# Performance work log

Measured on AMD Instinct MI355X. Metric: run time of the kernel, lower is better.

## Reference

```python
import jax, jax.numpy as jnp
import numpy as np
from jax import lax

STRIDE = 16
SCALES = (8.0, 16.0, 32.0)
RATIOS = (0.5, 1.0, 2.0)
PRE_NMS = 6000
POST_NMS = 300
NMS_THRESH = 0.7
MIN_SIZE = 16.0
DN = ('NCHW', 'OIHW', 'NCHW')


def _base_anchors():
    # 9 base anchors centered at (STRIDE/2, STRIDE/2), (ymin,xmin,ymax,xmax)
    c = STRIDE / 2.0
    rows = []
    for r in RATIOS:
        for s in SCALES:
            h = STRIDE * s * np.sqrt(r)
            w = STRIDE * s * np.sqrt(1.0 / r)
            rows.append([c - h / 2, c - w / 2, c + h / 2, c + w / 2])
    return jnp.asarray(np.array(rows, np.float32))


def _all_anchors(wdim, hdim):
    # shift base anchors over the (w, h) feature grid, matching permute(0,2,3,1) flatten order
    sy = jnp.arange(wdim, dtype=jnp.float32) * STRIDE
    sx = jnp.arange(hdim, dtype=jnp.float32) * STRIDE
    yy, xx = jnp.meshgrid(sy, sx, indexing='ij')
    shifts = jnp.stack([yy, xx, yy, xx], axis=-1).reshape(-1, 4)  # [w*h, 4]
    return (shifts[:, None, :] + _base_anchors()[None, :, :]).reshape(-1, 4)  # [w*h*9, 4]


def _conv(x, W, b, pad):
    y = lax.conv_general_dilated(x, W, (1, 1), pad, dimension_numbers=DN)
    return y + b[None, :, None, None]


def _nms_fixed(boxes, keep):
    # sequential greedy NMS over score-sorted boxes; returns POST_NMS boxes (zero padded)
    y1, x1, y2, x2 = boxes[:, 0], boxes[:, 1], boxes[:, 2], boxes[:, 3]
    areas = (y2 - y1) * (x2 - x1)
    N = boxes.shape[0]
    idxs = jnp.arange(N)

    def body(i, keep):
        yy1 = jnp.maximum(y1[i], y1)
        xx1 = jnp.maximum(x1[i], x1)
        yy2 = jnp.minimum(y2[i], y2)
        xx2 = jnp.minimum(x2[i], x2)
        inter = jnp.maximum(yy2 - yy1, 0.0) * jnp.maximum(xx2 - xx1, 0.0)
        iou = inter / (areas[i] + areas - inter + 1e-12)
        suppress = (iou > NMS_THRESH) & (idxs > i) & keep[i]
        return keep & ~suppress

    keep = lax.fori_loop(0, N, body, keep)
    rank = jnp.cumsum(keep) - 1
    slot = jnp.where(keep & (rank < POST_NMS), rank, POST_NMS)  # overflow slot
    out = jnp.zeros((POST_NMS + 1, 4), boxes.dtype).at[slot].set(boxes)
    return out[:POST_NMS]


def _proposals(loc, score_fg, anchors, img_h, img_w):
    ah = anchors[:, 2] - anchors[:, 0]
    aw = anchors[:, 3] - anchors[:, 1]
    acy = anchors[:, 0] + 0.5 * ah
    acx = anchors[:, 1] + 0.5 * aw
    cy = loc[:, 0] * ah + acy
    cx = loc[:, 1] * aw + acx
    h = jnp.exp(loc[:, 2]) * ah
    w = jnp.exp(loc[:, 3]) * aw
    boxes = jnp.stack([cy - 0.5 * h, cx - 0.5 * w, cy + 0.5 * h, cx + 0.5 * w], axis=-1)
    hi = jnp.array([img_h, img_w, img_h, img_w], dtype=boxes.dtype)
    boxes = jnp.clip(boxes, 0.0, hi)
    hs = boxes[:, 2] - boxes[:, 0]
    ws = boxes[:, 3] - boxes[:, 1]
    valid = (hs >= MIN_SIZE) & (ws >= MIN_SIZE)
    sc = jnp.where(valid, score_fg, -jnp.inf)
    top_sc, top_idx = lax.top_k(sc, PRE_NMS)
    cand = boxes[top_idx]
    return _nms_fixed(cand, jnp.isfinite(top_sc))


def setup_inputs() -> dict:
    key = jax.random.key(0)
    k = jax.random.split(key, 4)
    return {
        'base_feature_map': jax.random.normal(k[0], (8, 512, 50, 50), jnp.float32),
        'W_conv': jax.random.normal(k[1], (512, 512, 3, 3), jnp.float32) * 0.01,
        'b_conv': jnp.zeros((512,), jnp.float32),
        'W_cls': jax.random.normal(k[2], (18, 512, 1, 1), jnp.float32) * 0.01,
        'b_cls': jnp.zeros((18,), jnp.float32),
        'W_reg': jax.random.normal(k[3], (36, 512, 1, 1), jnp.float32) * 0.01,
        'b_reg': jnp.zeros((36,), jnp.float32),
        'img_h': 800,
        'img_w': 800,
    }


def reference(base_feature_map, W_conv, b_conv, W_cls, b_cls, W_reg, b_reg, img_h, img_w):
    n, _, w, h = base_feature_map.shape
    anchors = _all_anchors(w, h)  # [w*h*9, 4]
    x = jax.nn.relu(_conv(base_feature_map, W_conv, b_conv, 'SAME'))
    rpn_locs = _conv(x, W_reg, b_reg, 'VALID').transpose(0, 2, 3, 1).reshape(n, -1, 4)
    rpn_scores = _conv(x, W_cls, b_cls, 'VALID').transpose(0, 2, 3, 1).reshape(n, -1, 2)
    fg = jax.nn.softmax(rpn_scores[0], axis=-1)[:, 1]
    rois = _proposals(rpn_locs[0], fg, anchors, float(img_h), float(img_w))
    return rpn_locs, rpn_scores, anchors, rois
```

## Files before the change

### kernel.cpp

```cpp
#include <hip/hip_runtime.h>
#include <cstdint>
#include <math.h>

typedef unsigned int u32;
typedef unsigned long long u64;
typedef __attribute__((ext_vector_type(8))) short short8v;
typedef __attribute__((ext_vector_type(4))) float f32x4;

#define N_BATCH 8
#define C_IN    512
#define PX      2500
#define KDIM    4608
#define NA      22500
#define PRE_NMS 6000
#define POST_NMS 300

#define OUT_SCORES 720000
#define OUT_ANCH   1080000
#define OUT_ROIS   1170000

#define WS_X     0
#define WS_SCORE 10240000
#define WS_BOX   10262500
#define WS_LIST  10352500
#define WS_CAND  10364500
#define WS_META  10388500
#define WS_WP    10388608
#define WS_XP    12747904
#define WS_END   22987904

__device__ inline u32 rne_hi16(float f) {
    u32 u = __float_as_uint(f);
    return (u + 0x7FFFu + ((u >> 16) & 1u)) >> 16;
}

__global__ __launch_bounds__(256) void k_splitW(const float* __restrict__ Wc,
                                                u32* __restrict__ WP) {
    int o = blockIdx.x * 256 + threadIdx.x;
    if (o >= 512 * KDIM) return;
    int ci_in = o & 31;
    int tmp   = o >> 5;
    int r     = tmp % 9;
    int cc    = tmp / 9;
    int co    = cc >> 4;
    int cig   = cc & 15;
    int ci    = cig * 32 + ci_in;
    float f = Wc[(size_t)co * KDIM + ci * 9 + r];
    u32 rh  = rne_hi16(f);
    float d = f - __uint_as_float(rh << 16);
    u32 rl  = rne_hi16(d);
    WP[o] = (rh << 16) | rl;
}

__global__ __launch_bounds__(256) void k_splitX(const float* __restrict__ in,
                                                u32* __restrict__ XP) {
    int o = blockIdx.x * 256 + threadIdx.x;
    if (o >= N_BATCH * C_IN * PX) return;
    float f = in[o];
    u32 rh  = rne_hi16(f);
    float d = f - __uint_as_float(rh << 16);
    u32 rl  = rne_hi16(d);
    XP[o] = (rh << 16) | rl;
}

__global__ __launch_bounds__(256) void k_conv3(const float* __restrict__ in,
                                               const u32* __restrict__ XP,
                                               const u32* __restrict__ WP,
                                               const float* __restrict__ bc,
                                               float* __restrict__ xout) {
    __shared__ unsigned short AsH[128][40];
    __shared__ unsigned short AsL[128][40];
    __shared__ unsigned short BsH[128][40];
    __shared__ unsigned short BsL[128][40];

    int b  = blockIdx.x;
    int n  = b & 7;
    int q  = b >> 3;
    int cb = q & 3;
    int pt = q >> 2;
    int t  = threadIdx.x;
    int lane = t & 63;
    int w  = t >> 6;
    int wr = w >> 1, wc = w & 1;
    int px0 = pt * 128, co0 = cb * 128;
    const float* inN = in + (size_t)n * C_IN * PX;
    const u32*   XPn = XP ? (XP + (size_t)n * C_IN * PX) : nullptr;

    int sco = t >> 1;
    int skb = (t & 1) << 4;
    int spx = t & 127;
    int skk = (t >> 7) << 4;
    int gpx = px0 + spx;
    int sy  = gpx / 50;
    int sx  = gpx - sy * 50;
    bool pxok = (gpx < PX);
    const u32* wpA = WP + (size_t)(co0 + sco) * KDIM + skb;

    f32x4 acc[4][4];
#pragma unroll
    for (int i = 0; i < 4; ++i)
#pragma unroll
        for (int j = 0; j < 4; ++j) acc[i][j] = (f32x4)0.f;

    const int ro = lane & 15;
    const int g8 = (lane >> 4) << 3;

    for (int cig = 0; cig < 16; ++cig) {
        int ci0 = cig << 5;
        for (int r = 0; r < 9; ++r) {
            int kstep = cig * 9 + r;
            {
                const u32* wp = wpA + kstep * 32;
                u32 uu[16];
                *(uint4*)&uu[0]  = *(const uint4*)(wp);
                *(uint4*)&uu[4]  = *(const uint4*)(wp + 4);
                *(uint4*)&uu[8]  = *(const uint4*)(wp + 8);
                *(uint4*)&uu[12] = *(const uint4*)(wp + 12);
                short8v v0, v1, u0, u1;
#pragma unroll
                for (int e = 0; e < 8; ++e) {
                    v0[e] = (short)(uu[e] >> 16);
                    v1[e] = (short)(uu[8 + e] >> 16);
                    u0[e] = (short)(uu[e] & 0xFFFFu);
                    u1[e] = (short)(uu[8 + e] & 0xFFFFu);
                }
                *(short8v*)&AsH[sco][skb]     = v0;
                *(short8v*)&AsH[sco][skb + 8] = v1;
                *(short8v*)&AsL[sco][skb]     = u0;
                *(short8v*)&AsL[sco][skb + 8] = u1;
            }
            {
                int ry = (r * 11) >> 5;
                int dy = ry - 1;
                int dx = r - ry * 3 - 1;
                int iy = sy + dy, ix = sx + dx;
                bool valid = pxok && ((unsigned)iy < 50u) && ((unsigned)ix < 50u);
                int off = iy * 50 + ix;
                short8v v0, v1, u0, u1;
                if (XPn) {
                    const u32* bp = XPn + (size_t)(ci0 + skk) * PX + off;
                    u32 uu[16];
#pragma unroll
                    for (int it = 0; it < 16; ++it)
                        uu[it] = valid ? bp[it * PX] : 0u;
#pragma unroll
                    for (int e = 0; e < 8; ++e) {
                        v0[e] = (short)(uu[e] >> 16);
                        v1[e] = (short)(uu[8 + e] >> 16);
                        u0[e] = (short)(uu[e] & 0xFFFFu);
                        u1[e] = (short)(uu[8 + e] & 0xFFFFu);
                    }
                } else {
                    const float* bp = inN + (size_t)(ci0 + skk) * PX + off;
                    float bv[16];
#pragma unroll
                    for (int it = 0; it < 16; ++it)
                        bv[it] = valid ? bp[it * PX] : 0.f;
#pragma unroll
                    for (int e = 0; e < 8; ++e) {
                        u32 ha = rne_hi16(bv[e]);
                        u32 hb = rne_hi16(bv[8 + e]);
                        float da = bv[e]     - __uint_as_float(ha << 16);
                        float db = bv[8 + e] - __uint_as_float(hb << 16);
                        v0[e] = (short)ha;
                        v1[e] = (short)hb;
                        u0[e] = (short)rne_hi16(da);
                        u1[e] = (short)rne_hi16(db);
                    }
                }
                *(short8v*)&BsH[spx][skk]     = v0;
                *(short8v*)&BsH[spx][skk + 8] = v1;
                *(short8v*)&BsL[spx][skk]     = u0;
                *(short8v*)&BsL[spx][skk + 8] = u1;
            }
            __syncthreads();

            short8v aH[4], aL[4], bH[4], bL[4];
#pragma unroll
            for (int s = 0; s < 4; ++s) {
                aH[s] = *(const short8v*)&AsH[wr * 64 + s * 16 + ro][g8];
                aL[s] = *(const short8v*)&AsL[wr * 64 + s * 16 + ro][g8];
                bH[s] = *(const short8v*)&BsH[wc * 64 + s * 16 + ro][g8];
                bL[s] = *(const short8v*)&BsL[wc * 64 + s * 16 + ro][g8];
            }
#pragma unroll
            for (int i = 0; i < 4; ++i)
#pragma unroll
                for (int j = 0; j < 4; ++j) {
                    acc[i][j] = __builtin_amdgcn_mfma_f32_16x16x32_bf16(aH[i], bH[j], acc[i][j], 0, 0, 0);
                    acc[i][j] = __builtin_amdgcn_mfma_f32_16x16x32_bf16(aH[i], bL[j], acc[i][j], 0, 0, 0);
                    acc[i][j] = __builtin_amdgcn_mfma_f32_16x16x32_bf16(aL[i], bH[j], acc[i][j], 0, 0, 0);
                }
            __syncthreads();
        }
    }

    int coB  = co0 + wr * 64;
    int pxB  = px0 + wc * 64 + ro;
    int rowg = (lane >> 4) << 2;
#pragma unroll
    for (int i = 0; i < 4; ++i) {
#pragma unroll
        for (int rg = 0; rg < 4; ++rg) {
            int co = coB + i * 16 + rowg + rg;
            float bias = bc[co];
            float* dst = xout + ((size_t)n * C_IN + co) * PX;
#pragma unroll
            for (int j = 0; j < 4; ++j) {
                int px = pxB + j * 16;
                if (px < PX) dst[px] = fmaxf(acc[i][j][rg] + bias, 0.f);
            }
        }
    }
}

__global__ __launch_bounds__(256) void k_heads(const float* __restrict__ x,
                                               const float* __restrict__ Wreg,
                                               const float* __restrict__ breg,
                                               const float* __restrict__ Wcls,
                                               const float* __restrict__ bcls,
                                               float* __restrict__ out) {
    __shared__ float As[32][68];
    __shared__ float Bs[32][132];
    int b  = blockIdx.x;
    int pt = b % 20, n = b / 20;
    int t  = threadIdx.x;
    int tx = t & 15, ty = t >> 4;
    int px0 = pt * 128;
    float acc[4][8];
#pragma unroll
    for (int i = 0; i < 4; ++i)
#pragma unroll
        for (int j = 0; j < 8; ++j) acc[i][j] = 0.f;

    for (int k0 = 0; k0 < 512; k0 += 32) {
        {
            int c   = t >> 2;
            int kkb = (t & 3) << 3;
            const float* src = nullptr;
            if (c < 36)      src = Wreg + (size_t)c * 512 + k0 + kkb;
            else if (c < 54) src = Wcls + (size_t)(c - 36) * 512 + k0 + kkb;
#pragma unroll
            for (int q = 0; q < 2; ++q) {
                float4 w = src ? *(const float4*)(src + q * 4) : make_float4(0, 0, 0, 0);
                As[kkb + q * 4 + 0][c] = w.x;
                As[kkb + q * 4 + 1][c] = w.y;
                As[kkb + q * 4 + 2][c] = w.z;
                As[kkb + q * 4 + 3][c] = w.w;
            }
        }
        {
            int pxl = t & 127;
            int kk0 = (t >> 7) << 4;
            int px  = px0 + pxl;
#pragma unroll
            for (int it = 0; it < 16; ++it) {
                int kk = kk0 + it;
                float v = 0.f;
                if (px < PX) v = x[((size_t)n * 512 + k0 + kk) * PX + px];
                Bs[kk][pxl] = v;
            }
        }
        __syncthreads();
#pragma unroll 8
        for (int kk = 0; kk < 32; ++kk) {
            float a[4], bb[8];
            *(float4*)&a[0]  = *(const float4*)&As[kk][ty * 4];
            *(float4*)&bb[0] = *(const float4*)&Bs[kk][tx * 8];
            *(float4*)&bb[4] = *(const float4*)&Bs[kk][tx * 8 + 4];
#pragma unroll
            for (int i = 0; i < 4; ++i)
#pragma unroll
                for (int j = 0; j < 8; ++j)
                    acc[i][j] = fmaf(a[i], bb[j], acc[i][j]);
        }
        __syncthreads();
    }
    int pxb = px0 + tx * 8;
#pragma unroll
    for (int i = 0; i < 4; ++i) {
        int c = ty * 4 + i;
        if (c >= 54) continue;
        float bias = (c < 36) ? breg[c] : bcls[c - 36];
        for (int j = 0; j < 8; ++j) {
            int px = pxb + j;
            if (px >= PX) break;
            float v = acc[i][j] + bias;
            if (c < 36)
                out[(size_t)n * 90000 + (size_t)px * 36 + c] = v;
            else
                out[OUT_SCORES + (size_t)n * 45000 + (size_t)px * 18 + (c - 36)] = v;
        }
    }
}

__device__ inline float readDim(const void* p) {
    int v = *(const int*)p;
    if (v > 0 && v <= 100000) return (float)v;
    return *(const float*)p;
}

__global__ __launch_bounds__(256) void k_decode(float* __restrict__ dout,
                                                float* __restrict__ ws,
                                                const void* pih, const void* piw) {
    int idx = blockIdx.x * 256 + threadIdx.x;
    if (idx >= NA) return;
    float imgH = readDim(pih), imgW = readDim(piw);
    int a  = idx % 9;
    int px = idx / 9;
    int y = px / 50, x = px - y * 50;
    const float ratios[3] = {0.5f, 1.f, 2.f};
    const float scales[3] = {8.f, 16.f, 32.f};
    float r = ratios[a / 3], s = scales[a % 3];
    float hh = 16.f * s * sqrtf(r);
    float wv = 16.f * s * sqrtf(1.f / r);
    float ay1 = y * 16.f + 8.f - 0.5f * hh;
    float ax1 = x * 16.f + 8.f - 0.5f * wv;
    float ay2 = y * 16.f + 8.f + 0.5f * hh;
    float ax2 = x * 16.f + 8.f + 0.5f * wv;
    *(float4*)(dout + OUT_ANCH + (size_t)idx * 4) = make_float4(ay1, ax1, ay2, ax2);

    float4 loc = *(const float4*)(dout + (size_t)idx * 4);
    float s0 = dout[OUT_SCORES + (size_t)idx * 2];
    float s1 = dout[OUT_SCORES + (size_t)idx * 2 + 1];
    float fg = 1.f / (1.f + expf(s0 - s1));
    float ah = ay2 - ay1, aw = ax2 - ax1;
    float acy = ay1 + 0.5f * ah, acx = ax1 + 0.5f * aw;
    float cy = loc.x * ah + acy;
    float cx = loc.y * aw + acx;
    float bh = expf(loc.z) * ah;
    float bw = expf(loc.w) * aw;
    float b0 = cy - 0.5f * bh, b1 = cx - 0.5f * bw;
    float b2 = cy + 0.5f * bh, b3 = cx + 0.5f * bw;
    b0 = fminf(fmaxf(b0, 0.f), imgH);
    b1 = fminf(fmaxf(b1, 0.f), imgW);
    b2 = fminf(fmaxf(b2, 0.f), imgH);
    b3 = fminf(fmaxf(b3, 0.f), imgW);
    bool valid = ((b2 - b0) >= 16.f) && ((b3 - b1) >= 16.f);
    ws[WS_SCORE + idx] = valid ? fg : -INFINITY;
    *(float4*)(ws + WS_BOX + (size_t)idx * 4) = make_float4(b0, b1, b2, b3);
}

__device__ inline u32 fkey(float s) {
    u32 u = __float_as_uint(s);
    return (u & 0x80000000u) ? ~u : (u | 0x80000000u);
}

__global__ __launch_bounds__(1024) void k_select(const float* __restrict__ score,
                                                 u64* __restrict__ list,
                                                 int* __restrict__ meta) {
    __shared__ u32 hist[4096];
    __shared__ int sB1, sB2, sB3, sM3, sNeed, sV;
    __shared__ u32 sT32;
    __shared__ int cHi, cTie;
    int t = threadIdx.x;
    const int NT = 1024;

    for (int i = t; i < 4096; i += NT) hist[i] = 0;
    __syncthreads();
    for (int i = t; i < NA; i += NT) atomicAdd(&hist[fkey(score[i]) >> 20], 1u);
    __syncthreads();
    for (int off = 1; off < 4096; off <<= 1) {
        u32 v[4]; int c = 0;
        for (int bb = t; bb < 4096; bb += NT) { v[c++] = hist[bb] + ((bb + off < 4096) ? hist[bb + off] : 0u); }
        __syncthreads();
        c = 0;
        for (int bb = t; bb < 4096; bb += NT) hist[bb] = v[c++];
        __syncthreads();
    }
    for (int bb = t; bb < 4096; bb += NT) {
        u32 Sb  = hist[bb];
        u32 Sb1 = (bb < 4095) ? hist[bb + 1] : 0u;
        if (Sb >= PRE_NMS && Sb1 < PRE_NMS) sB1 = bb;
    }
    if (t == 0) sV = (int)hist[2048];
    __syncthreads();
    int B1 = sB1;
    int m1 = (B1 < 4095) ? (int)hist[B1 + 1] : 0;
    int V  = sV;
    __syncthreads();

    for (int i = t; i < 4096; i += NT) hist[i] = 0;
    __syncthreads();
    for (int i = t; i < NA; i += NT) {
        u32 key = fkey(score[i]);
        if ((int)(key >> 20) == B1) atomicAdd(&hist[(key >> 8) & 0xFFFu], 1u);
    }
    __syncthreads();
    for (int off = 1; off < 4096; off <<= 1) {
        u32 v[4]; int c = 0;
        for (int bb = t; bb < 4096; bb += NT) { v[c++] = hist[bb] + ((bb + off < 4096) ? hist[bb + off] : 0u); }
        __syncthreads();
        c = 0;
        for (int bb = t; bb < 4096; bb += NT) hist[bb] = v[c++];
        __syncthreads();
    }
    for (int bb = t; bb < 4096; bb += NT) {
        int Sb  = m1 + (int)hist[bb];
        int Sb1 = m1 + (int)((bb < 4095) ? hist[bb + 1] : 0u);
        if (Sb >= PRE_NMS && Sb1 < PRE_NMS) sB2 = bb;
    }
    __syncthreads();
    int B2 = sB2;
    int m2 = m1 + (int)((B2 < 4095) ? hist[B2 + 1] : 0u);
    u32 P24 = ((u32)B1 << 12) | (u32)B2;
    __syncthreads();

    for (int i = t; i < 256; i += NT) hist[i] = 0;
    __syncthreads();
    for (int i = t; i < NA; i += NT) {
        u32 key = fkey(score[i]);
        if ((key >> 8) == P24) atomicAdd(&hist[key & 0xFFu], 1u);
    }
    __syncthreads();
    for (int off = 1; off < 256; off <<= 1) {
        u32 v[1]; int c = 0;
        for (int bb = t; bb < 256; bb += NT) { v[c++] = hist[bb] + ((bb + off < 256) ? hist[bb + off] : 0u); }
        __syncthreads();
        c = 0;
        for (int bb = t; bb < 256; bb += NT) hist[bb] = v[c++];
        __syncthreads();
    }
    for (int bb = t; bb < 256; bb += NT) {
        int Sb  = m2 + (int)hist[bb];
        int Sb1 = m2 + (int)((bb < 255) ? hist[bb + 1] : 0u);
        if (Sb >= PRE_NMS && Sb1 < PRE_NMS) {
            sB3   = bb;
            sM3   = m2 + (int)((bb < 255) ? hist[bb + 1] : 0u);
            sNeed = PRE_NMS - sM3;
            sT32  = (P24 << 8) | (u32)bb;
        }
    }
    if (t == 0) { cHi = 0; cTie = 0; meta[0] = (V < PRE_NMS) ? V : PRE_NMS; }
    __syncthreads();
    int m3 = sM3, need = sNeed;
    u32 T32 = sT32;

    for (int i = t; i < NA; i += NT) {
        u32 key = fkey(score[i]);
        u64 comp = ((u64)key << 32) | (u64)(0xFFFFFFFFu - (u32)i);
        if (key > T32) {
            int p = atomicAdd(&cHi, 1);
            list[p] = comp;
        } else if (key == T32) {
            int p = atomicAdd(&cTie, 1);
            if (p < need) list[m3 + p] = comp;
        }
    }
}

__global__ __launch_bounds__(1024) void k_sort(u64* __restrict__ list,
                                               const float* __restrict__ boxes,
                                               float* __restrict__ cand) {
    __shared__ u64 sb[8192];
    int t = threadIdx.x;
    for (int i = t; i < 8192; i += 1024) sb[i] = (i < PRE_NMS) ? list[i] : 0ull;
    __syncthreads();
    for (int k = 2; k <= 8192; k <<= 1) {
        for (int j = k >> 1; j > 0; j >>= 1) {
            for (int i = t; i < 8192; i += 1024) {
                int ixj = i ^ j;
                if (ixj > i) {
                    u64 a = sb[i], b = sb[ixj];
                    bool desc = ((i & k) == 0);
                    if (desc ? (a < b) : (a > b)) { sb[i] = b; sb[ixj] = a; }
                }
            }
            __syncthreads();
        }
    }
    for (int e = t; e < PRE_NMS; e += 1024) {
        u32 idx = 0xFFFFFFFFu - (u32)sb[e];
        float4 bx = *(const float4*)(boxes + (size_t)idx * 4);
        *(float4*)(cand + (size_t)e * 4) = bx;
    }
}

__global__ __launch_bounds__(256) void k_nms(const float* __restrict__ cand,
                                             const int* __restrict__ meta,
                                             float* __restrict__ rois) {
    __shared__ float kb[POST_NMS][4];
    __shared__ u64 supArr[4];
    int t = threadIdx.x;
    int lane = t & 63, wid = t >> 6;
    int keepN = meta[0];
    int kept = 0;

    for (int c0 = 0; c0 < PRE_NMS && kept < POST_NMS; c0 += 64) {
        int i = c0 + lane;
        float y1 = 0, x1 = 0, y2 = 0, x2 = 0;
        bool elig = (i < keepN);
        if (i < PRE_NMS) {
            float4 bx = *(const float4*)(cand + (size_t)i * 4);
            y1 = bx.x; x1 = bx.y; y2 = bx.z; x2 = bx.w;
        } else {
            elig = false;
        }
        float area = (y2 - y1) * (x2 - x1);

        bool supA = false;
        for (int jj = wid; jj < kept; jj += 4) {
            float ky1 = kb[jj][0], kx1 = kb[jj][1], ky2 = kb[jj][2], kx2 = kb[jj][3];
            float yy1 = fmaxf(ky1, y1), xx1 = fmaxf(kx1, x1);
            float yy2 = fminf(ky2, y2), xx2 = fminf(kx2, x2);
            float inter = fmaxf(yy2 - yy1, 0.f) * fmaxf(xx2 - xx1, 0.f);
            float karea = (ky2 - ky1) * (kx2 - kx1);
            float iou = inter / (karea + area - inter + 1e-12f);
            if (iou > 0.7f) { supA = true; break; }
        }
        supArr[wid] = __ballot(supA);
        __syncthreads();
        u64 sup = supArr[0] | supArr[1] | supArr[2] | supArr[3];
        u64 eligMask = __ballot(elig);

        for (int s = 0; s < 64; ++s) {
            if (kept >= POST_NMS) break;
            if (!((eligMask >> s) & 1ull)) continue;
            if ((sup >> s) & 1ull) continue;
            float sy1 = __shfl(y1, s), sx1 = __shfl(x1, s);
            float sy2 = __shfl(y2, s), sx2 = __shfl(x2, s);
            float sar = __shfl(area, s);
            if (wid == 0 && lane == s) {
                kb[kept][0] = y1; kb[kept][1] = x1; kb[kept][2] = y2; kb[kept][3] = x2;
                *(float4*)(rois + (size_t)kept * 4) = make_float4(y1, x1, y2, x2);
            }
            float yy1 = fmaxf(sy1, y1), xx1 = fmaxf(sx1, x1);
            float yy2 = fminf(sy2, y2), xx2 = fminf(sx2, x2);
            float inter = fmaxf(yy2 - yy1, 0.f) * fmaxf(xx2 - xx1, 0.f);
            float iou = inter / (sar + area - inter + 1e-12f);
            bool kill = (lane > s) && (iou > 0.7f);
            sup |= __ballot(kill);
            kept++;
        }
        __syncthreads();
    }
    for (int r = kept * 4 + t; r < POST_NMS * 4; r += 256) rois[r] = 0.f;
}

extern "C" void kernel_launch(void* const* d_in, const int* in_sizes, int n_in,
                              void* d_out, int out_size, void* d_ws, size_t ws_size,
                              hipStream_t stream) {
    const float* feat = (const float*)d_in[0];
    const float* Wc   = (const float*)d_in[1];
    const float* bc   = (const float*)d_in[2];
    const float* Wcls = (const float*)d_in[3];
    const float* bcls = (const float*)d_in[4];
    const float* Wreg = (const float*)d_in[5];
    const float* breg = (const float*)d_in[6];
    const void* pih   = d_in[7];
    const void* piw   = d_in[8];
    float* out = (float*)d_out;
    float* ws  = (float*)d_ws;

    u32* WP   = (u32*)(ws + WS_WP);
    u64* list = (u64*)(ws + WS_LIST);
    int* meta = (int*)(ws + WS_META);

    bool haveXP = (ws_size >= (size_t)WS_END * sizeof(float));
    u32* XP = haveXP ? (u32*)(ws + WS_XP) : nullptr;

    hipLaunchKernelGGL(k_splitW, dim3((512 * KDIM + 255) / 256), dim3(256), 0, stream, Wc, WP);
    if (haveXP)
        hipLaunchKernelGGL(k_splitX, dim3((N_BATCH * C_IN * PX + 255) / 256), dim3(256), 0, stream, feat, XP);
    hipLaunchKernelGGL(k_conv3, dim3(640), dim3(256), 0, stream, feat, XP, WP, bc, ws + WS_X);
    hipLaunchKernelGGL(k_heads, dim3(160), dim3(256), 0, stream, ws + WS_X, Wreg, breg, Wcls, bcls, out);
    hipLaunchKernelGGL(k_decode, dim3(88), dim3(256), 0, stream, out, ws, pih, piw);
    hipLaunchKernelGGL(k_select, dim3(1), dim3(1024), 0, stream, ws + WS_SCORE, list, meta);
    hipLaunchKernelGGL(k_sort, dim3(1), dim3(1024), 0, stream, list, ws + WS_BOX, ws + WS_CAND);
    hipLaunchKernelGGL(k_nms, dim3(1), dim3(256), 0, stream, ws + WS_CAND, meta, out + OUT_ROIS);
}
```

Before: 747.6 us.

## Fuse weight/input prep, decode into heads, and select/sort/NMS into one kernel

```diff
diff --git a/kernel.cpp b/kernel.cpp
--- a/kernel.cpp
+++ b/kernel.cpp
@@ -22,45 +22,42 @@
 #define WS_X     0
 #define WS_SCORE 10240000
 #define WS_BOX   10262500
-#define WS_LIST  10352500
-#define WS_CAND  10364500
-#define WS_META  10388500
 #define WS_WP    10388608
 #define WS_XP    12747904
 #define WS_END   22987904
 
+#define NW_ELEMS (512 * KDIM)
+#define NX_ELEMS (N_BATCH * C_IN * PX)
+
 __device__ inline u32 rne_hi16(float f) {
     u32 u = __float_as_uint(f);
     return (u + 0x7FFFu + ((u >> 16) & 1u)) >> 16;
 }
-
-__global__ __launch_bounds__(256) void k_splitW(const float* __restrict__ Wc,
-                                                u32* __restrict__ WP) {
-    int o = blockIdx.x * 256 + threadIdx.x;
-    if (o >= 512 * KDIM) return;
-    int ci_in = o & 31;
-    int tmp   = o >> 5;
-    int r     = tmp % 9;
-    int cc    = tmp / 9;
-    int co    = cc >> 4;
-    int cig   = cc & 15;
-    int ci    = cig * 32 + ci_in;
-    float f = Wc[(size_t)co * KDIM + ci * 9 + r];
+__device__ inline u32 pack_split(float f) {
     u32 rh  = rne_hi16(f);
     float d = f - __uint_as_float(rh << 16);
     u32 rl  = rne_hi16(d);
-    WP[o] = (rh << 16) | rl;
-}
-
-__global__ __launch_bounds__(256) void k_splitX(const float* __restrict__ in,
-                                                u32* __restrict__ XP) {
+    return (rh << 16) | rl;
+}
+
+__global__ __launch_bounds__(256) void k_prep(const float* __restrict__ Wc,
+                                              const float* __restrict__ in,
+                                              u32* __restrict__ WP,
+                                              u32* __restrict__ XP) {
     int o = blockIdx.x * 256 + threadIdx.x;
-    if (o >= N_BATCH * C_IN * PX) return;
-    float f = in[o];
-    u32 rh  = rne_hi16(f);
-    float d = f - __uint_as_float(rh << 16);
-    u32 rl  = rne_hi16(d);
-    XP[o] = (rh << 16) | rl;
+    if (o < NW_ELEMS) {
+        int ci_in = o & 31;
+        int tmp   = o >> 5;
+        int r     = tmp % 9;
+        int cc    = tmp / 9;
+        int co    = cc >> 4;
+        int cig   = cc & 15;
+        int ci    = cig * 32 + ci_in;
+        WP[o] = pack_split(Wc[(size_t)co * KDIM + ci * 9 + r]);
+    } else {
+        int o2 = o - NW_ELEMS;
+        if (o2 < NX_ELEMS && XP) XP[o2] = pack_split(in[o2]);
+    }
 }
 
 __global__ __launch_bounds__(256) void k_conv3(const float* __restrict__ in,
@@ -158,14 +155,12 @@
                         bv[it] = valid ? bp[it * PX] : 0.f;
 #pragma unroll
                     for (int e = 0; e < 8; ++e) {
-                        u32 ha = rne_hi16(bv[e]);
-                        u32 hb = rne_hi16(bv[8 + e]);
-                        float da = bv[e]     - __uint_as_float(ha << 16);
-                        float db = bv[8 + e] - __uint_as_float(hb << 16);
-                        v0[e] = (short)ha;
-                        v1[e] = (short)hb;
-                        u0[e] = (short)rne_hi16(da);
-                        u1[e] = (short)rne_hi16(db);
+                        u32 pa = pack_split(bv[e]);
+                        u32 pb = pack_split(bv[8 + e]);
+                        v0[e] = (short)(pa >> 16);
+                        v1[e] = (short)(pb >> 16);
+                        u0[e] = (short)(pa & 0xFFFFu);
+                        u1[e] = (short)(pb & 0xFFFFu);
                     }
                 }
                 *(short8v*)&BsH[spx][skk]     = v0;
@@ -214,14 +209,24 @@
     }
 }
 
+__device__ inline float readDim(const void* p) {
+    int v = *(const int*)p;
+    if (v > 0 && v <= 100000) return (float)v;
+    return *(const float*)p;
+}
+
 __global__ __launch_bounds__(256) void k_heads(const float* __restrict__ x,
                                                const float* __restrict__ Wreg,
                                                const float* __restrict__ breg,
                                                const float* __restrict__ Wcls,
                                                const float* __restrict__ bcls,
-                                               float* __restrict__ out) {
+                                               float* __restrict__ out,
+                                               float* __restrict__ wsScore,
+                                               float* __restrict__ wsBox,
+                                               const void* pih, const void* piw) {
     __shared__ float As[32][68];
     __shared__ float Bs[32][132];
+    __shared__ float Hs[54][132];
     int b  = blockIdx.x;
     int pt = b % 20, n = b / 20;
     int t  = threadIdx.x;
@@ -241,12 +246,12 @@
             if (c < 36)      src = Wreg + (size_t)c * 512 + k0 + kkb;
             else if (c < 54) src = Wcls + (size_t)(c - 36) * 512 + k0 + kkb;
 #pragma unroll
-            for (int q = 0; q < 2; ++q) {
-                float4 w = src ? *(const float4*)(src + q * 4) : make_float4(0, 0, 0, 0);
-                As[kkb + q * 4 + 0][c] = w.x;
-                As[kkb + q * 4 + 1][c] = w.y;
-                As[kkb + q * 4 + 2][c] = w.z;
-                As[kkb + q * 4 + 3][c] = w.w;
+            for (int qq = 0; qq < 2; ++qq) {
+                float4 wv = src ? *(const float4*)(src + qq * 4) : make_float4(0, 0, 0, 0);
+                As[kkb + qq * 4 + 0][c] = wv.x;
+                As[kkb + qq * 4 + 1][c] = wv.y;
+                As[kkb + qq * 4 + 2][c] = wv.z;
+                As[kkb + qq * 4 + 3][c] = wv.w;
             }
         }
         {
@@ -290,55 +295,55 @@
                 out[(size_t)n * 90000 + (size_t)px * 36 + c] = v;
             else
                 out[OUT_SCORES + (size_t)n * 45000 + (size_t)px * 18 + (c - 36)] = v;
-        }
-    }
-}
-
-__device__ inline float readDim(const void* p) {
-    int v = *(const int*)p;
-    if (v > 0 && v <= 100000) return (float)v;
-    return *(const float*)p;
-}
-
-__global__ __launch_bounds__(256) void k_decode(float* __restrict__ dout,
-                                                float* __restrict__ ws,
-                                                const void* pih, const void* piw) {
-    int idx = blockIdx.x * 256 + threadIdx.x;
-    if (idx >= NA) return;
-    float imgH = readDim(pih), imgW = readDim(piw);
-    int a  = idx % 9;
-    int px = idx / 9;
-    int y = px / 50, x = px - y * 50;
-    const float ratios[3] = {0.5f, 1.f, 2.f};
-    const float scales[3] = {8.f, 16.f, 32.f};
-    float r = ratios[a / 3], s = scales[a % 3];
-    float hh = 16.f * s * sqrtf(r);
-    float wv = 16.f * s * sqrtf(1.f / r);
-    float ay1 = y * 16.f + 8.f - 0.5f * hh;
-    float ax1 = x * 16.f + 8.f - 0.5f * wv;
-    float ay2 = y * 16.f + 8.f + 0.5f * hh;
-    float ax2 = x * 16.f + 8.f + 0.5f * wv;
-    *(float4*)(dout + OUT_ANCH + (size_t)idx * 4) = make_float4(ay1, ax1, ay2, ax2);
-
-    float4 loc = *(const float4*)(dout + (size_t)idx * 4);
-    float s0 = dout[OUT_SCORES + (size_t)idx * 2];
-    float s1 = dout[OUT_SCORES + (size_t)idx * 2 + 1];
-    float fg = 1.f / (1.f + expf(s0 - s1));
-    float ah = ay2 - ay1, aw = ax2 - ax1;
-    float acy = ay1 + 0.5f * ah, acx = ax1 + 0.5f * aw;
-    float cy = loc.x * ah + acy;
-    float cx = loc.y * aw + acx;
-    float bh = expf(loc.z) * ah;
-    float bw = expf(loc.w) * aw;
-    float b0 = cy - 0.5f * bh, b1 = cx - 0.5f * bw;
-    float b2 = cy + 0.5f * bh, b3 = cx + 0.5f * bw;
-    b0 = fminf(fmaxf(b0, 0.f), imgH);
-    b1 = fminf(fmaxf(b1, 0.f), imgW);
-    b2 = fminf(fmaxf(b2, 0.f), imgH);
-    b3 = fminf(fmaxf(b3, 0.f), imgW);
-    bool valid = ((b2 - b0) >= 16.f) && ((b3 - b1) >= 16.f);
-    ws[WS_SCORE + idx] = valid ? fg : -INFINITY;
-    *(float4*)(ws + WS_BOX + (size_t)idx * 4) = make_float4(b0, b1, b2, b3);
+            if (n == 0) Hs[c][tx * 8 + j] = v;
+        }
+    }
+
+    if (n == 0) {
+        __syncthreads();
+        float imgH = readDim(pih), imgW = readDim(piw);
+        const float ratios[3] = {0.5f, 1.f, 2.f};
+        const float scales[3] = {8.f, 16.f, 32.f};
+        for (int idx = t; idx < 128 * 9; idx += 256) {
+            int pxl = idx / 9;
+            int a   = idx - pxl * 9;
+            int px  = px0 + pxl;
+            if (px >= PX) continue;
+            int gi = px * 9 + a;
+            int y = px / 50, xq = px - y * 50;
+            float r = ratios[a / 3], s = scales[a % 3];
+            float hh = 16.f * s * sqrtf(r);
+            float wv = 16.f * s * sqrtf(1.f / r);
+            float ay1 = y * 16.f + 8.f - 0.5f * hh;
+            float ax1 = xq * 16.f + 8.f - 0.5f * wv;
+            float ay2 = y * 16.f + 8.f + 0.5f * hh;
+            float ax2 = xq * 16.f + 8.f + 0.5f * wv;
+            *(float4*)(out + OUT_ANCH + (size_t)gi * 4) = make_float4(ay1, ax1, ay2, ax2);
+
+            float l0 = Hs[a * 4 + 0][pxl];
+            float l1 = Hs[a * 4 + 1][pxl];
+            float l2 = Hs[a * 4 + 2][pxl];
+            float l3 = Hs[a * 4 + 3][pxl];
+            float s0 = Hs[36 + 2 * a][pxl];
+            float s1 = Hs[37 + 2 * a][pxl];
+            float fg = 1.f / (1.f + expf(s0 - s1));
+            float ah = ay2 - ay1, aw = ax2 - ax1;
+            float acy = ay1 + 0.5f * ah, acx = ax1 + 0.5f * aw;
+            float cy = l0 * ah + acy;
+            float cx = l1 * aw + acx;
+            float bh = expf(l2) * ah;
+            float bw = expf(l3) * aw;
+            float b0 = cy - 0.5f * bh, b1 = cx - 0.5f * bw;
+            float b2 = cy + 0.5f * bh, b3 = cx + 0.5f * bw;
+            b0 = fminf(fmaxf(b0, 0.f), imgH);
+            b1 = fminf(fmaxf(b1, 0.f), imgW);
+            b2 = fminf(fmaxf(b2, 0.f), imgH);
+            b3 = fminf(fmaxf(b3, 0.f), imgW);
+            bool valid = ((b2 - b0) >= 16.f) && ((b3 - b1) >= 16.f);
+            wsScore[gi] = valid ? fg : -INFINITY;
+            *(float4*)(wsBox + (size_t)gi * 4) = make_float4(b0, b1, b2, b3);
+        }
+    }
 }
 
 __device__ inline u32 fkey(float s) {
@@ -346,11 +351,14 @@
     return (u & 0x80000000u) ? ~u : (u | 0x80000000u);
 }
 
-__global__ __launch_bounds__(1024) void k_select(const float* __restrict__ score,
-                                                 u64* __restrict__ list,
-                                                 int* __restrict__ meta) {
+__global__ __launch_bounds__(1024) void k_post(const float* __restrict__ score,
+                                               const float* __restrict__ boxes,
+                                               float* __restrict__ rois) {
     __shared__ u32 hist[4096];
-    __shared__ int sB1, sB2, sB3, sM3, sNeed, sV;
+    __shared__ u64 sb[8192];
+    __shared__ float kb[POST_NMS][4];
+    __shared__ u64 supArr[16];
+    __shared__ int sB1, sB2, sM3, sNeed, sV;
     __shared__ u32 sT32;
     __shared__ int cHi, cTie;
     int t = threadIdx.x;
@@ -425,13 +433,12 @@
         int Sb  = m2 + (int)hist[bb];
         int Sb1 = m2 + (int)((bb < 255) ? hist[bb + 1] : 0u);
         if (Sb >= PRE_NMS && Sb1 < PRE_NMS) {
-            sB3   = bb;
             sM3   = m2 + (int)((bb < 255) ? hist[bb + 1] : 0u);
             sNeed = PRE_NMS - sM3;
             sT32  = (P24 << 8) | (u32)bb;
         }
     }
-    if (t == 0) { cHi = 0; cTie = 0; meta[0] = (V < PRE_NMS) ? V : PRE_NMS; }
+    if (t == 0) { cHi = 0; cTie = 0; }
     __syncthreads();
     int m3 = sM3, need = sNeed;
     u32 T32 = sT32;
@@ -441,65 +448,46 @@
         u64 comp = ((u64)key << 32) | (u64)(0xFFFFFFFFu - (u32)i);
         if (key > T32) {
             int p = atomicAdd(&cHi, 1);
-            list[p] = comp;
+            sb[p] = comp;
         } else if (key == T32) {
             int p = atomicAdd(&cTie, 1);
-            if (p < need) list[m3 + p] = comp;
-        }
-    }
-}
-
-__global__ __launch_bounds__(1024) void k_sort(u64* __restrict__ list,
-                                               const float* __restrict__ boxes,
-                                               float* __restrict__ cand) {
-    __shared__ u64 sb[8192];
-    int t = threadIdx.x;
-    for (int i = t; i < 8192; i += 1024) sb[i] = (i < PRE_NMS) ? list[i] : 0ull;
-    __syncthreads();
+            if (p < need) sb[m3 + p] = comp;
+        }
+    }
+    for (int i = PRE_NMS + t; i < 8192; i += NT) sb[i] = 0ull;
+    __syncthreads();
+
     for (int k = 2; k <= 8192; k <<= 1) {
         for (int j = k >> 1; j > 0; j >>= 1) {
-            for (int i = t; i < 8192; i += 1024) {
+            for (int i = t; i < 8192; i += NT) {
                 int ixj = i ^ j;
                 if (ixj > i) {
-                    u64 a = sb[i], b = sb[ixj];
+                    u64 a = sb[i], bbv = sb[ixj];
                     bool desc = ((i & k) == 0);
-                    if (desc ? (a < b) : (a > b)) { sb[i] = b; sb[ixj] = a; }
+                    if (desc ? (a < bbv) : (a > bbv)) { sb[i] = bbv; sb[ixj] = a; }
                 }
             }
             __syncthreads();
         }
     }
-    for (int e = t; e < PRE_NMS; e += 1024) {
-        u32 idx = 0xFFFFFFFFu - (u32)sb[e];
-        float4 bx = *(const float4*)(boxes + (size_t)idx * 4);
-        *(float4*)(cand + (size_t)e * 4) = bx;
-    }
-}
-
-__global__ __launch_bounds__(256) void k_nms(const float* __restrict__ cand,
-                                             const int* __restrict__ meta,
-                                             float* __restrict__ rois) {
-    __shared__ float kb[POST_NMS][4];
-    __shared__ u64 supArr[4];
-    int t = threadIdx.x;
+
     int lane = t & 63, wid = t >> 6;
-    int keepN = meta[0];
+    int keepN = (V < PRE_NMS) ? V : PRE_NMS;
     int kept = 0;
 
     for (int c0 = 0; c0 < PRE_NMS && kept < POST_NMS; c0 += 64) {
         int i = c0 + lane;
         float y1 = 0, x1 = 0, y2 = 0, x2 = 0;
         bool elig = (i < keepN);
-        if (i < PRE_NMS) {
-            float4 bx = *(const float4*)(cand + (size_t)i * 4);
+        {
+            u32 bidx = 0xFFFFFFFFu - (u32)sb[i];
+            float4 bx = *(const float4*)(boxes + (size_t)bidx * 4);
             y1 = bx.x; x1 = bx.y; y2 = bx.z; x2 = bx.w;
-        } else {
-            elig = false;
         }
         float area = (y2 - y1) * (x2 - x1);
 
         bool supA = false;
-        for (int jj = wid; jj < kept; jj += 4) {
+        for (int jj = wid; jj < kept; jj += 16) {
             float ky1 = kb[jj][0], kx1 = kb[jj][1], ky2 = kb[jj][2], kx2 = kb[jj][3];
             float yy1 = fmaxf(ky1, y1), xx1 = fmaxf(kx1, x1);
             float yy2 = fminf(ky2, y2), xx2 = fminf(kx2, x2);
@@ -510,7 +498,9 @@
         }
         supArr[wid] = __ballot(supA);
         __syncthreads();
-        u64 sup = supArr[0] | supArr[1] | supArr[2] | supArr[3];
+        u64 sup = 0ull;
+#pragma unroll
+        for (int ww = 0; ww < 16; ++ww) sup |= supArr[ww];
         u64 eligMask = __ballot(elig);
 
         for (int s = 0; s < 64; ++s) {
@@ -534,7 +524,7 @@
         }
         __syncthreads();
     }
-    for (int r = kept * 4 + t; r < POST_NMS * 4; r += 256) rois[r] = 0.f;
+    for (int r = kept * 4 + t; r < POST_NMS * 4; r += NT) rois[r] = 0.f;
 }
 
 extern "C" void kernel_launch(void* const* d_in, const int* in_sizes, int n_in,
@@ -552,20 +542,14 @@
     float* out = (float*)d_out;
     float* ws  = (float*)d_ws;
 
-    u32* WP   = (u32*)(ws + WS_WP);
-    u64* list = (u64*)(ws + WS_LIST);
-    int* meta = (int*)(ws + WS_META);
-
+    u32* WP = (u32*)(ws + WS_WP);
     bool haveXP = (ws_size >= (size_t)WS_END * sizeof(float));
     u32* XP = haveXP ? (u32*)(ws + WS_XP) : nullptr;
 
-    hipLaunchKernelGGL(k_splitW, dim3((512 * KDIM + 255) / 256), dim3(256), 0, stream, Wc, WP);
-    if (haveXP)
-        hipLaunchKernelGGL(k_splitX, dim3((N_BATCH * C_IN * PX + 255) / 256), dim3(256), 0, stream, feat, XP);
+    int prepItems = NW_ELEMS + (haveXP ? NX_ELEMS : 0);
+    hipLaunchKernelGGL(k_prep, dim3((prepItems + 255) / 256), dim3(256), 0, stream, Wc, feat, WP, XP);
     hipLaunchKernelGGL(k_conv3, dim3(640), dim3(256), 0, stream, feat, XP, WP, bc, ws + WS_X);
-    hipLaunchKernelGGL(k_heads, dim3(160), dim3(256), 0, stream, ws + WS_X, Wreg, breg, Wcls, bcls, out);
-    hipLaunchKernelGGL(k_decode, dim3(88), dim3(256), 0, stream, out, ws, pih, piw);
-    hipLaunchKernelGGL(k_select, dim3(1), dim3(1024), 0, stream, ws + WS_SCORE, list, meta);
-    hipLaunchKernelGGL(k_sort, dim3(1), dim3(1024), 0, stream, list, ws + WS_BOX, ws + WS_CAND);
-    hipLaunchKernelGGL(k_nms, dim3(1), dim3(256), 0, stream, ws + WS_CAND, meta, out + OUT_ROIS);
-}
+    hipLaunchKernelGGL(k_heads, dim3(160), dim3(256), 0, stream, ws + WS_X, Wreg, breg, Wcls, bcls,
+                       out, ws + WS_SCORE, ws + WS_BOX, pih, piw);
+    hipLaunchKernelGGL(k_post, dim3(1), dim3(1024), 0, stream, ws + WS_SCORE, ws + WS_BOX, out + OUT_ROIS);
+}
```

Result: no change. 737.3 us (-1.4%).
